# Kernel optimization log

Hardware: AMD Instinct MI355X
Metric: run time of the kernel (lower is better)

The kernel has to match this reference:

```python
import jax, jax.numpy as jnp
import numpy as np

DIM = 1024
N_HEADS = 16
HEAD_DIM = DIM // N_HEADS
D_LATENT = 256
B, T = 1, 4096


def setup_inputs() -> dict:
    key = jax.random.key(0)
    ks = jax.random.split(key, 6)
    s = 0.02
    return {
        "x": jax.random.normal(ks[0], (B, T, DIM), dtype=jnp.float32),
        "W_DKV": jax.random.normal(ks[1], (DIM, D_LATENT), dtype=jnp.float32) * s,
        "W_UK": jax.random.normal(ks[2], (D_LATENT, DIM), dtype=jnp.float32) * s,
        "W_UV": jax.random.normal(ks[3], (D_LATENT, DIM), dtype=jnp.float32) * s,
        "W_UQ": jax.random.normal(ks[4], (DIM, DIM), dtype=jnp.float32) * s,
        "W_O": jax.random.normal(ks[5], (DIM, DIM), dtype=jnp.float32) * s,
    }


def reference(x, W_DKV, W_UK, W_UV, W_UQ, W_O):
    b, t, d = x.shape
    h, hd = N_HEADS, HEAD_DIM
    # low-rank latent KV projection
    c_kv = x @ W_DKV                                   # (b, t, d_latent)
    k = (c_kv @ W_UK).reshape(b, t, h, hd)             # (b, t, h, hd)
    v = (c_kv @ W_UV).reshape(b, t, h, hd)
    q = (x @ W_UQ).reshape(b, t, h, hd)
    scale = 1.0 / jnp.sqrt(jnp.asarray(hd, x.dtype))
    scores = jnp.einsum("bqhd,bkhd->bhqk", q, k) * scale   # (b, h, t, t)
    causal = jnp.tril(jnp.ones((t, t), dtype=bool))
    scores = jnp.where(causal, scores, jnp.asarray(-jnp.inf, scores.dtype))
    probs = jax.nn.softmax(scores, axis=-1)            # dropout is eval-mode identity
    ctx = jnp.einsum("bhqk,bkhd->bqhd", probs, v).reshape(b, t, d)
    return ctx @ W_O
```

## Files before the change

### kernel.cpp

```cpp
#include <hip/hip_runtime.h>
#include <hip/hip_bf16.h>
#include <stdint.h>

#define T_SEQ 4096
#define DIMX 1024
#define NH 16
#define HD 64
#define DLAT 256

typedef __bf16 bf16x8 __attribute__((ext_vector_type(8)));
typedef float floatx4 __attribute__((ext_vector_type(4)));

#define MFMA(a, b, c) __builtin_amdgcn_mfma_f32_16x16x32_bf16(a, b, c, 0, 0, 0)

__device__ inline void gload_lds16(const __bf16* g, __bf16* l) {
  __builtin_amdgcn_global_load_lds(
      (const __attribute__((address_space(1))) uint32_t*)g,
      (__attribute__((address_space(3))) uint32_t*)l, 16, 0, 0);
}

__global__ __launch_bounds__(256) void prep_kernel(
    const float* __restrict__ x, const float* __restrict__ wdkv,
    const float* __restrict__ wuk, const float* __restrict__ wuv,
    const float* __restrict__ wuq, const float* __restrict__ wo,
    __bf16* __restrict__ x_bf, __bf16* __restrict__ wt_dkv,
    __bf16* __restrict__ wt_uk, __bf16* __restrict__ wt_uv,
    __bf16* __restrict__ wt_uq, __bf16* __restrict__ wt_o) {
  int id = blockIdx.x;
  if (id < 2048) {
    int i = id * 256 + threadIdx.x;
    const float4* p = (const float4*)x;
    float4 a = p[2 * i], b = p[2 * i + 1];
    bf16x8 r = {(__bf16)a.x, (__bf16)a.y, (__bf16)a.z, (__bf16)a.w,
                (__bf16)b.x, (__bf16)b.y, (__bf16)b.z, (__bf16)b.w};
    *(bf16x8*)(x_bf + 8 * (size_t)i) = r;
    return;
  }
  int t = id - 2048;
  const float* in;
  __bf16* out;
  int R, C, lt;
  if (t < 64)       { in = wdkv; out = wt_dkv; R = 1024; C = 256;  lt = t; }
  else if (t < 128) { in = wuk;  out = wt_uk;  R = 256;  C = 1024; lt = t - 64; }
  else if (t < 192) { in = wuv;  out = wt_uv;  R = 256;  C = 1024; lt = t - 128; }
  else if (t < 448) { in = wuq;  out = wt_uq;  R = 1024; C = 1024; lt = t - 192; }
  else              { in = wo;   out = wt_o;   R = 1024; C = 1024; lt = t - 448; }
  __shared__ __bf16 tls[64][65];
  int tpr = C >> 6;
  int r0 = (lt / tpr) * 64, c0 = (lt % tpr) * 64;
  int tid = threadIdx.x;
#pragma unroll
  for (int i = 0; i < 16; i++) {
    int idx = tid + i * 256;
    int r = idx >> 6, c = idx & 63;
    tls[r][c] = (__bf16)in[(size_t)(r0 + r) * C + c0 + c];
  }
  __syncthreads();
#pragma unroll
  for (int i = 0; i < 16; i++) {
    int idx = tid + i * 256;
    int rr = idx & 63, cc = idx >> 6;
    out[(size_t)(c0 + cc) * R + r0 + rr] = tls[rr][cc];
  }
}

#define BUFE 4096

__global__ __launch_bounds__(256) void gemm_a128(const __bf16* __restrict__ A,
                                                 const __bf16* __restrict__ B1,
                                                 const __bf16* __restrict__ B2,
                                                 __bf16* __restrict__ C1,
                                                 __bf16* __restrict__ C2) {
  __shared__ __attribute__((aligned(16))) __bf16 Al[2][BUFE];
  __shared__ __attribute__((aligned(16))) __bf16 Bl[2][BUFE];
  int tid = threadIdx.x;
  int w = tid >> 6, lane = tid & 63;
  int quad = lane >> 4, l16 = lane & 15;
  int mw = w & 1, nw = w >> 1;
  int bx = blockIdx.x, m0 = blockIdx.y * 128;
  const __bf16* Bt;
  __bf16* C;
  int n0, N;
  float sc;
  if (bx < 2) { Bt = B1; C = C1; n0 = bx * 128; N = DLAT; sc = 1.0f; }
  else        { Bt = B2; C = C2; n0 = (bx - 2) * 128; N = DIMX; sc = 0.125f; }
  const int K = DIMX;
  int arow = w * 32 + (lane >> 2), acol = (lane & 3) << 3;

  floatx4 acc[4][4];
#pragma unroll
  for (int i = 0; i < 4; i++)
#pragma unroll
    for (int j = 0; j < 4; j++) acc[i][j] = (floatx4){0.f, 0.f, 0.f, 0.f};

  for (int k0 = 0; k0 < K; k0 += 64) {
#pragma unroll
    for (int kh = 0; kh < 2; kh++)
#pragma unroll
      for (int j = 0; j < 2; j++) {
        gload_lds16(A + (size_t)(m0 + arow + j * 16) * K + k0 + kh * 32 + acol,
                    &Al[kh][(w * 32 + j * 16) * 32]);
        gload_lds16(Bt + (size_t)(n0 + arow + j * 16) * K + k0 + kh * 32 + acol,
                    &Bl[kh][(w * 32 + j * 16) * 32]);
      }
    __syncthreads();
#pragma unroll
    for (int kh = 0; kh < 2; kh++) {
      bf16x8 af[4], bfr[4];
#pragma unroll
      for (int mt = 0; mt < 4; mt++)
        af[mt] =
            *(const bf16x8*)&Al[kh][(mw * 64 + mt * 16 + l16) * 32 + quad * 8];
#pragma unroll
      for (int nt = 0; nt < 4; nt++)
        bfr[nt] =
            *(const bf16x8*)&Bl[kh][(nw * 64 + nt * 16 + l16) * 32 + quad * 8];
#pragma unroll
      for (int mt = 0; mt < 4; mt++)
#pragma unroll
        for (int nt = 0; nt < 4; nt++)
          acc[mt][nt] = MFMA(af[mt], bfr[nt], acc[mt][nt]);
    }
    __syncthreads();
  }
#pragma unroll
  for (int mt = 0; mt < 4; mt++)
#pragma unroll
    for (int nt = 0; nt < 4; nt++)
#pragma unroll
      for (int r = 0; r < 4; r++) {
        int row = m0 + mw * 64 + mt * 16 + quad * 4 + r;
        int col = n0 + nw * 64 + nt * 16 + l16;
        C[(size_t)row * N + col] = (__bf16)(acc[mt][nt][r] * sc);
      }
}

__global__ __launch_bounds__(256) void gemm_kv128(const __bf16* __restrict__ A,
                                                  const __bf16* __restrict__ Bk,
                                                  const __bf16* __restrict__ Bv,
                                                  __bf16* __restrict__ k,
                                                  __bf16* __restrict__ vt) {
  __shared__ __attribute__((aligned(16))) __bf16 Al[2][BUFE];
  __shared__ __attribute__((aligned(16))) __bf16 Bl[2][BUFE];
  __shared__ __attribute__((aligned(16))) __bf16 tw[4][64 * 72];
  int tid = threadIdx.x;
  int w = tid >> 6, lane = tid & 63;
  int quad = lane >> 4, l16 = lane & 15;
  int mw = w & 1, nw = w >> 1;
  int bx = blockIdx.x, m0 = blockIdx.y * 128;
  bool is_k = (bx < 8);
  const __bf16* Bt = is_k ? Bk : Bv;
  int n0 = (is_k ? bx : bx - 8) * 128;
  const int K = DLAT;
  int arow = w * 32 + (lane >> 2), acol = (lane & 3) << 3;

  floatx4 acc[4][4];
#pragma unroll
  for (int i = 0; i < 4; i++)
#pragma unroll
    for (int j = 0; j < 4; j++) acc[i][j] = (floatx4){0.f, 0.f, 0.f, 0.f};

  for (int k0 = 0; k0 < K; k0 += 64) {
#pragma unroll
    for (int kh = 0; kh < 2; kh++)
#pragma unroll
      for (int j = 0; j < 2; j++) {
        gload_lds16(A + (size_t)(m0 + arow + j * 16) * K + k0 + kh * 32 + acol,
                    &Al[kh][(w * 32 + j * 16) * 32]);
        gload_lds16(Bt + (size_t)(n0 + arow + j * 16) * K + k0 + kh * 32 + acol,
                    &Bl[kh][(w * 32 + j * 16) * 32]);
      }
    __syncthreads();
#pragma unroll
    for (int kh = 0; kh < 2; kh++) {
      bf16x8 af[4], bfr[4];
#pragma unroll
      for (int mt = 0; mt < 4; mt++)
        af[mt] =
            *(const bf16x8*)&Al[kh][(mw * 64 + mt * 16 + l16) * 32 + quad * 8];
#pragma unroll
      for (int nt = 0; nt < 4; nt++)
        bfr[nt] =
            *(const bf16x8*)&Bl[kh][(nw * 64 + nt * 16 + l16) * 32 + quad * 8];
#pragma unroll
      for (int mt = 0; mt < 4; mt++)
#pragma unroll
        for (int nt = 0; nt < 4; nt++)
          acc[mt][nt] = MFMA(af[mt], bfr[nt], acc[mt][nt]);
    }
    __syncthreads();
  }
  if (is_k) {
#pragma unroll
    for (int mt = 0; mt < 4; mt++)
#pragma unroll
      for (int nt = 0; nt < 4; nt++)
#pragma unroll
        for (int r = 0; r < 4; r++) {
          int row = m0 + mw * 64 + mt * 16 + quad * 4 + r;
          int col = n0 + nw * 64 + nt * 16 + l16;
          k[(size_t)row * DIMX + col] = (__bf16)acc[mt][nt][r];
        }
  } else {
#pragma unroll
    for (int mt = 0; mt < 4; mt++)
#pragma unroll
      for (int nt = 0; nt < 4; nt++)
#pragma unroll
        for (int r = 0; r < 4; r++)
          tw[w][(nt * 16 + l16) * 72 + mt * 16 + quad * 4 + r] =
              (__bf16)acc[mt][nt][r];
    int cbase = lane >> 3, chunk = lane & 7;
#pragma unroll
    for (int i = 0; i < 8; i++) {
      int c = cbase + i * 8;
      bf16x8 v8 = *(const bf16x8*)&tw[w][c * 72 + chunk * 8];
      *(bf16x8*)&vt[(size_t)(n0 + nw * 64 + c) * T_SEQ + m0 + mw * 64 +
                    chunk * 8] = v8;
    }
  }
}

__global__ __launch_bounds__(256) void gemm_f128(const __bf16* __restrict__ A,
                                                 const __bf16* __restrict__ Bt,
                                                 float* __restrict__ C) {
  __shared__ __attribute__((aligned(16))) __bf16 Al[2][BUFE];
  __shared__ __attribute__((aligned(16))) __bf16 Bl[2][BUFE];
  int tid = threadIdx.x;
  int w = tid >> 6, lane = tid & 63;
  int quad = lane >> 4, l16 = lane & 15;
  int mw = w & 1, nw = w >> 1;
  int n0 = blockIdx.x * 128, m0 = blockIdx.y * 128;
  const int K = DIMX, N = DIMX;
  int arow = w * 32 + (lane >> 2), acol = (lane & 3) << 3;

  floatx4 acc[4][4];
#pragma unroll
  for (int i = 0; i < 4; i++)
#pragma unroll
    for (int j = 0; j < 4; j++) acc[i][j] = (floatx4){0.f, 0.f, 0.f, 0.f};

  for (int k0 = 0; k0 < K; k0 += 64) {
#pragma unroll
    for (int kh = 0; kh < 2; kh++)
#pragma unroll
      for (int j = 0; j < 2; j++) {
        gload_lds16(A + (size_t)(m0 + arow + j * 16) * K + k0 + kh * 32 + acol,
                    &Al[kh][(w * 32 + j * 16) * 32]);
        gload_lds16(Bt + (size_t)(n0 + arow + j * 16) * K + k0 + kh * 32 + acol,
                    &Bl[kh][(w * 32 + j * 16) * 32]);
      }
    __syncthreads();
#pragma unroll
    for (int kh = 0; kh < 2; kh++) {
      bf16x8 af[4], bfr[4];
#pragma unroll
      for (int mt = 0; mt < 4; mt++)
        af[mt] =
            *(const bf16x8*)&Al[kh][(mw * 64 + mt * 16 + l16) * 32 + quad * 8];
#pragma unroll
      for (int nt = 0; nt < 4; nt++)
        bfr[nt] =
            *(const bf16x8*)&Bl[kh][(nw * 64 + nt * 16 + l16) * 32 + quad * 8];
#pragma unroll
      for (int mt = 0; mt < 4; mt++)
#pragma unroll
        for (int nt = 0; nt < 4; nt++)
          acc[mt][nt] = MFMA(af[mt], bfr[nt], acc[mt][nt]);
    }
    __syncthreads();
  }
#pragma unroll
  for (int mt = 0; mt < 4; mt++)
#pragma unroll
    for (int nt = 0; nt < 4; nt++)
#pragma unroll
      for (int r = 0; r < 4; r++) {
        int row = m0 + mw * 64 + mt * 16 + quad * 4 + r;
        int col = n0 + nw * 64 + nt * 16 + l16;
        C[(size_t)row * N + col] = acc[mt][nt][r];
      }
}

#define PST 72
__global__ __launch_bounds__(512, 4) void mla_attn5(const __bf16* __restrict__ Q,
                                                    const __bf16* __restrict__ Kg,
                                                    const __bf16* __restrict__ Vt,
                                                    __bf16* __restrict__ ctx) {
  __shared__ __attribute__((aligned(16))) __bf16 Kl[2][64 * 64];
  __shared__ __attribute__((aligned(16))) __bf16 Vl[2][64 * 64];
  __shared__ __attribute__((aligned(16))) __bf16 Pl[128 * PST];
  int tid = threadIdx.x;
  int wave = tid >> 6, lane = tid & 63;
  int quad = lane >> 4, l16 = lane & 15;
  int wq = wave & 3;
  bool isA = (wave < 4);
  int h = blockIdx.y;
  int qa = (h & 8) ? (31 - blockIdx.x) : blockIdx.x;
  int qb = 63 - qa;
  int myqt = isA ? qa : qb;
  int myq0 = myqt * 64;
  int srow = tid >> 3, pos = tid & 7;
  int gco = pos << 3;
  int sw = ((pos ^ (srow & 7)) << 3);
  int swr = srow * 64 + sw;

  *(bf16x8*)&Pl[srow * PST + gco] =
      *(const bf16x8*)&Q[(size_t)(qa * 64 + srow) * DIMX + h * HD + gco];
  *(bf16x8*)&Pl[(64 + srow) * PST + gco] =
      *(const bf16x8*)&Q[(size_t)(qb * 64 + srow) * DIMX + h * HD + gco];
  *(bf16x8*)&Kl[0][swr] =
      *(const bf16x8*)&Kg[(size_t)srow * DIMX + h * HD + gco];
  *(bf16x8*)&Vl[0][swr] =
      *(const bf16x8*)&Vt[(size_t)(h * HD + srow) * T_SEQ + gco];
  __syncthreads();
  int fr = (wave * 16 + l16) * PST;
  bf16x8 qf0 = *(const bf16x8*)&Pl[fr + quad * 8];
  bf16x8 qf1 = *(const bf16x8*)&Pl[fr + 32 + quad * 8];

  int c0s = ((quad ^ (l16 & 7)) << 3);
  int c1s = (((4 + quad) ^ (l16 & 7)) << 3);

  floatx4 o[4];
  float l_i[4];
#pragma unroll
  for (int i = 0; i < 4; i++) {
    o[i] = (floatx4){0.f, 0.f, 0.f, 0.f};
    l_i[i] = 0.f;
  }

  for (int kt = 0; kt <= qb; kt++) {
    int cur = kt & 1, nxt = cur ^ 1;
    bool pre = (kt < qb);
    bf16x8 kpre, vpre;
    if (pre) {
      int k0n = (kt + 1) * 64;
      kpre = *(const bf16x8*)&Kg[(size_t)(k0n + srow) * DIMX + h * HD + gco];
      vpre = *(const bf16x8*)&Vt[(size_t)(h * HD + srow) * T_SEQ + k0n + gco];
    }
    if (!isA || kt <= qa) {
      const __bf16* Kc = Kl[cur];
      const __bf16* Vc = Vl[cur];
      floatx4 s[4];
#pragma unroll
      for (int ct = 0; ct < 4; ct++) {
        int rb = (ct * 16 + l16) * 64;
        bf16x8 kf0 = *(const bf16x8*)&Kc[rb + c0s];
        bf16x8 kf1 = *(const bf16x8*)&Kc[rb + c1s];
        floatx4 z = (floatx4){0.f, 0.f, 0.f, 0.f};
        z = MFMA(qf0, kf0, z);
        z = MFMA(qf1, kf1, z);
        s[ct] = z;
      }
      bool diag = (kt == myqt);
#pragma unroll
      for (int ct = 0; ct < 4; ct++)
#pragma unroll
        for (int r = 0; r < 4; r++) {
          float p = __expf(s[ct][r]);
          if (diag && (ct * 16 + l16 > wq * 16 + quad * 4 + r)) p = 0.f;
          l_i[r] += p;
          Pl[(wave * 16 + quad * 4 + r) * PST + ct * 16 + l16] = (__bf16)p;
        }
      bf16x8 pf0 = *(const bf16x8*)&Pl[fr + quad * 8];
      bf16x8 pf1 = *(const bf16x8*)&Pl[fr + 32 + quad * 8];
#pragma unroll
      for (int dt = 0; dt < 4; dt++) {
        int rb = (dt * 16 + l16) * 64;
        bf16x8 vf0 = *(const bf16x8*)&Vc[rb + c0s];
        bf16x8 vf1 = *(const bf16x8*)&Vc[rb + c1s];
        o[dt] = MFMA(pf0, vf0, o[dt]);
        o[dt] = MFMA(pf1, vf1, o[dt]);
      }
    }
    if (pre) {
      *(bf16x8*)&Kl[nxt][swr] = kpre;
      *(bf16x8*)&Vl[nxt][swr] = vpre;
    }
    __syncthreads();
  }

#pragma unroll
  for (int off = 1; off < 16; off <<= 1)
#pragma unroll
    for (int r = 0; r < 4; r++) l_i[r] += __shfl_xor(l_i[r], off, 64);

#pragma unroll
  for (int dt = 0; dt < 4; dt++)
#pragma unroll
    for (int r = 0; r < 4; r++) {
      float val = o[dt][r] / l_i[r];
      int row = myq0 + wq * 16 + quad * 4 + r;
      int col = h * HD + dt * 16 + l16;
      ctx[(size_t)row * DIMX + col] = (__bf16)val;
    }
}

extern "C" void kernel_launch(void* const* d_in, const int* in_sizes, int n_in,
                              void* d_out, int out_size, void* d_ws,
                              size_t ws_size, hipStream_t stream) {
  const float* x = (const float*)d_in[0];
  const float* wdkv = (const float*)d_in[1];
  const float* wuk = (const float*)d_in[2];
  const float* wuv = (const float*)d_in[3];
  const float* wuq = (const float*)d_in[4];
  const float* wo = (const float*)d_in[5];
  float* out = (float*)d_out;

  __bf16* ws = (__bf16*)d_ws;
  __bf16* x_bf = ws;
  __bf16* q = x_bf + (size_t)T_SEQ * DIMX;
  __bf16* k = q + (size_t)T_SEQ * DIMX;
  __bf16* vt = k + (size_t)T_SEQ * DIMX;
  __bf16* ctx = vt + (size_t)T_SEQ * DIMX;
  __bf16* ckv = ctx + (size_t)T_SEQ * DIMX;
  __bf16* wt_dkv = ckv + (size_t)T_SEQ * DLAT;
  __bf16* wt_uk = wt_dkv + (size_t)DLAT * DIMX;
  __bf16* wt_uv = wt_uk + (size_t)DIMX * DLAT;
  __bf16* wt_uq = wt_uv + (size_t)DIMX * DLAT;
  __bf16* wt_o = wt_uq + (size_t)DIMX * DIMX;

  dim3 blk(256);
  prep_kernel<<<dim3(2752), blk, 0, stream>>>(x, wdkv, wuk, wuv, wuq, wo, x_bf,
                                              wt_dkv, wt_uk, wt_uv, wt_uq, wt_o);
  gemm_a128<<<dim3(10, T_SEQ / 128), blk, 0, stream>>>(x_bf, wt_dkv, wt_uq,
                                                       ckv, q);
  gemm_kv128<<<dim3(16, T_SEQ / 128), blk, 0, stream>>>(ckv, wt_uk, wt_uv, k,
                                                        vt);
  mla_attn5<<<dim3(32, NH), dim3(512), 0, stream>>>(q, k, vt, ctx);
  gemm_f128<<<dim3(DIMX / 128, T_SEQ / 128), blk, 0, stream>>>(ctx, wt_o, out);
}
```

Measured before the change: 214.2 us.

## Transpose QK^T MFMA output, fold log2e into Q scale, pack P writes

The QK^T MFMA operands are swapped so each lane holds four consecutive key columns for one query row. This lets the probabilities be written to LDS as packed 4-element bf16 stores instead of scalar stores, and the row sums collapse to a single per-lane accumulator reduced with two shuffles. log2(e) is folded into the Q projection scale so the softmax can use the native exp2 instruction. The MFMA phases are also wrapped in s_setprio, and the final division becomes a reciprocal multiply. The causal mask condition is transposed to match the new layout, so correctness depends on getting those indices right.

```diff
diff --git a/kernel.cpp b/kernel.cpp
--- a/kernel.cpp
+++ b/kernel.cpp
@@ -9,6 +9,7 @@
 #define DLAT 256
 
 typedef __bf16 bf16x8 __attribute__((ext_vector_type(8)));
+typedef __bf16 bf16x4 __attribute__((ext_vector_type(4)));
 typedef float floatx4 __attribute__((ext_vector_type(4)));
 
 #define MFMA(a, b, c) __builtin_amdgcn_mfma_f32_16x16x32_bf16(a, b, c, 0, 0, 0)
@@ -83,7 +84,8 @@
   int n0, N;
   float sc;
   if (bx < 2) { Bt = B1; C = C1; n0 = bx * 128; N = DLAT; sc = 1.0f; }
-  else        { Bt = B2; C = C2; n0 = (bx - 2) * 128; N = DIMX; sc = 0.125f; }
+  else        { Bt = B2; C = C2; n0 = (bx - 2) * 128; N = DIMX;
+                sc = 0.125f * 1.44269504088896340736f; }
   const int K = DIMX;
   int arow = w * 32 + (lane >> 2), acol = (lane & 3) << 3;
 
@@ -322,12 +324,9 @@
   int c1s = (((4 + quad) ^ (l16 & 7)) << 3);
 
   floatx4 o[4];
-  float l_i[4];
-#pragma unroll
-  for (int i = 0; i < 4; i++) {
-    o[i] = (floatx4){0.f, 0.f, 0.f, 0.f};
-    l_i[i] = 0.f;
-  }
+  float lsum = 0.f;
+#pragma unroll
+  for (int i = 0; i < 4; i++) o[i] = (floatx4){0.f, 0.f, 0.f, 0.f};
 
   for (int kt = 0; kt <= qb; kt++) {
     int cur = kt & 1, nxt = cur ^ 1;
@@ -342,28 +341,35 @@
       const __bf16* Kc = Kl[cur];
       const __bf16* Vc = Vl[cur];
       floatx4 s[4];
+      __builtin_amdgcn_s_setprio(1);
 #pragma unroll
       for (int ct = 0; ct < 4; ct++) {
         int rb = (ct * 16 + l16) * 64;
         bf16x8 kf0 = *(const bf16x8*)&Kc[rb + c0s];
         bf16x8 kf1 = *(const bf16x8*)&Kc[rb + c1s];
         floatx4 z = (floatx4){0.f, 0.f, 0.f, 0.f};
-        z = MFMA(qf0, kf0, z);
-        z = MFMA(qf1, kf1, z);
+        z = MFMA(kf0, qf0, z);
+        z = MFMA(kf1, qf1, z);
         s[ct] = z;
       }
+      __builtin_amdgcn_s_setprio(0);
       bool diag = (kt == myqt);
 #pragma unroll
-      for (int ct = 0; ct < 4; ct++)
+      for (int ct = 0; ct < 4; ct++) {
+        float p0[4];
 #pragma unroll
         for (int r = 0; r < 4; r++) {
-          float p = __expf(s[ct][r]);
-          if (diag && (ct * 16 + l16 > wq * 16 + quad * 4 + r)) p = 0.f;
-          l_i[r] += p;
-          Pl[(wave * 16 + quad * 4 + r) * PST + ct * 16 + l16] = (__bf16)p;
+          float p = __builtin_amdgcn_exp2f(s[ct][r]);
+          if (diag && (ct * 16 + quad * 4 + r > wq * 16 + l16)) p = 0.f;
+          lsum += p;
+          p0[r] = p;
         }
+        bf16x4 pk = {(__bf16)p0[0], (__bf16)p0[1], (__bf16)p0[2], (__bf16)p0[3]};
+        *(bf16x4*)&Pl[(wave * 16 + l16) * PST + ct * 16 + quad * 4] = pk;
+      }
       bf16x8 pf0 = *(const bf16x8*)&Pl[fr + quad * 8];
       bf16x8 pf1 = *(const bf16x8*)&Pl[fr + 32 + quad * 8];
+      __builtin_amdgcn_s_setprio(1);
 #pragma unroll
       for (int dt = 0; dt < 4; dt++) {
         int rb = (dt * 16 + l16) * 64;
@@ -372,6 +378,7 @@
         o[dt] = MFMA(pf0, vf0, o[dt]);
         o[dt] = MFMA(pf1, vf1, o[dt]);
       }
+      __builtin_amdgcn_s_setprio(0);
     }
     if (pre) {
       *(bf16x8*)&Kl[nxt][swr] = kpre;
@@ -380,16 +387,17 @@
     __syncthreads();
   }
 
-#pragma unroll
-  for (int off = 1; off < 16; off <<= 1)
-#pragma unroll
-    for (int r = 0; r < 4; r++) l_i[r] += __shfl_xor(l_i[r], off, 64);
+  lsum += __shfl_xor(lsum, 16, 64);
+  lsum += __shfl_xor(lsum, 32, 64);
+  float inv[4];
+#pragma unroll
+  for (int r = 0; r < 4; r++) inv[r] = 1.0f / __shfl(lsum, quad * 4 + r, 16);
 
 #pragma unroll
   for (int dt = 0; dt < 4; dt++)
 #pragma unroll
     for (int r = 0; r < 4; r++) {
-      float val = o[dt][r] / l_i[r];
+      float val = o[dt][r] * inv[r];
       int row = myq0 + wq * 16 + quad * 4 + r;
       int col = h * HD + dt * 16 + l16;
       ctx[(size_t)row * DIMX + col] = (__bf16)val;
```

New measurement: 198.8 us. 7.2% less time.
